# Performance work log

Measured on AMD Instinct MI355X. Metric: run time of the kernel, lower is better.

The kernel has to match this reference:

```python
import jax, jax.numpy as jnp
import numpy as np

N_PTS = 262144      # 512x512 coordinate grid
N_HEADS = 16
HID = 256
N_HID_LAYERS = 3
IN_F = 2
OUT_F = 3
PE_L = 10                  # NeRF positional-encoding frequencies
PE_DIM = 2 * IN_F * PE_L   # sin+cos per freq per coord = 40
CAP = N_PTS // N_HEADS     # balanced partition: points per head


def positional_encoding(x):
    # x: [..., IN_F] -> [..., PE_DIM]
    freqs = (2.0 ** jnp.arange(PE_L, dtype=x.dtype)) * jnp.pi          # [L]
    ang = x[..., None, :] * freqs[:, None]                              # [..., L, IN_F]
    pe = jnp.concatenate([jnp.sin(ang), jnp.cos(ang)], axis=-1)        # [..., L, 2*IN_F]
    return pe.reshape(*x.shape[:-1], PE_DIM)


def setup_inputs() -> dict:
    key = jax.random.key(0)
    ks = jax.random.split(key, 5)
    # Balanced random segment map (equivalent to the module's segment_weight),
    # converted to the static routing table the torch loop recomputes each step:
    # head_idx[h] = where(segment_weight == h)
    rng = np.random.default_rng(0)
    seg = rng.permutation(np.arange(N_PTS) % N_HEADS)
    head_idx = np.stack([np.where(seg == h)[0] for h in range(N_HEADS)]).astype(np.int32)  # [H, CAP]

    coords = jax.random.uniform(ks[0], (1, N_PTS, IN_F), minval=-1.0, maxval=1.0)

    def he(k, shape, fan_in):
        return jax.random.normal(k, shape, dtype=jnp.float32) * np.float32(np.sqrt(2.0 / fan_in))

    W_in = he(ks[1], (N_HEADS, PE_DIM, HID), PE_DIM)
    b_in = jnp.zeros((N_HEADS, HID), jnp.float32)
    W_hid = he(ks[2], (N_HEADS, N_HID_LAYERS, HID, HID), HID)
    b_hid = jnp.zeros((N_HEADS, N_HID_LAYERS, HID), jnp.float32)
    W_out = he(ks[3], (N_HEADS, HID, OUT_F), HID)
    b_out = jnp.zeros((N_HEADS, OUT_F), jnp.float32)

    return dict(coords=coords, head_idx=jnp.asarray(head_idx),
                W_in=W_in, b_in=b_in, W_hid=W_hid, b_hid=b_hid,
                W_out=W_out, b_out=b_out)


def reference(coords, head_idx, W_in, b_in, W_hid, b_hid, W_out, b_out):
    # --- dispatch: gather each head's points (torch: coords[:, index, :]) ---
    coords_h = coords[0][head_idx]                                      # [H, CAP, IN_F]
    # --- per-head MLP (relu_MLP with positional embedding) ---
    h = jax.nn.relu(jnp.einsum('hcd,hdf->hcf', positional_encoding(coords_h), W_in)
                    + b_in[:, None, :])                                 # [H, CAP, HID]
    for l in range(N_HID_LAYERS):
        h = jax.nn.relu(jnp.einsum('hcf,hfg->hcg', h, W_hid[:, l])
                        + b_hid[:, l, None, :])
    out_h = jnp.einsum('hcf,hfo->hco', h, W_out) + b_out[:, None, :]    # [H, CAP, OUT_F]
    # --- combine: scatter per-head outputs back (torch: output_final[0, index, :] = out) ---
    out_final = jnp.zeros((1, N_PTS, OUT_F), coords.dtype)
    out_final = out_final.at[0, head_idx.reshape(-1)].set(out_h.reshape(-1, OUT_F))
    return (out_final, coords)
```

## Files before the change

kernel.cpp:

```cpp
#include <hip/hip_runtime.h>

typedef unsigned short u16;
typedef unsigned int   u32;
typedef __bf16  bf16x8 __attribute__((ext_vector_type(8)));
typedef float   f32x16 __attribute__((ext_vector_type(16)));

#define CAP      16384
#define L0Q_ELS  3072
#define L0_ELS   (4*L0Q_ELS)
#define HID_ELS  (256*256)
#define OUT_ELS  (16*512)
#define HEAD_WS  (L0_ELS + 3*HID_ELS + OUT_ELS)
#define HID_OFF  L0_ELS
#define OUT_OFF  (L0_ELS + 3*HID_ELS)
#define HEAD_CH  (HEAD_WS/8)

union F8 { u32 u[4]; bf16x8 v; };

__device__ __forceinline__ u16 f2b(float f) {
  u32 u = __float_as_uint(f); u += 0x7fffu + ((u >> 16) & 1u); return (u16)(u >> 16);
}
__device__ __forceinline__ u32 packbf2(float a, float b) {
  u32 ua = __float_as_uint(a); ua += 0x7fffu + ((ua >> 16) & 1u);
  u32 ub = __float_as_uint(b); ub += 0x7fffu + ((ub >> 16) & 1u);
  return (ua >> 16) | (ub & 0xffff0000u);
}

__device__ __forceinline__ f32x16 mfma16(bf16x8 a, bf16x8 b, f32x16 c) {
  return __builtin_amdgcn_mfma_f32_32x32x16_bf16(a, b, c, 0, 0, 0);
}

__device__ __forceinline__ void stage_async(const u16* __restrict__ g, short* l,
                                            int bytes, int tid) {
  for (int base = tid * 16; base < bytes; base += 4096)
    __builtin_amdgcn_global_load_lds(
        (const __attribute__((address_space(1))) u32*)((const char*)g + base),
        (__attribute__((address_space(3))) u32*)((char*)l + base), 16, 0, 0);
}

__device__ __forceinline__ bf16x8 fragL0(const short* sl, int i, int t, int lane) {
  return *(const bf16x8*)((const char*)sl + ((i*3 + t) << 10) + (lane << 4));
}
__device__ __forceinline__ bf16x8 fragH(const short* sl, int i, int t, int lane) {
  return *(const bf16x8*)((const char*)sl + ((i*16 + t) << 10) + (lane << 4));
}

__device__ __forceinline__ void load_bias_raw(const float* b, int r, int hh, float4 o[4]) {
#pragma unroll
  for (int g = 0; g < 4; ++g) o[g] = *(const float4*)(b + 32*r + 8*g + 4*hh);
}
__device__ __forceinline__ f32x16 bias_to_acc(const float4 raw[4]) {
  f32x16 a;
#pragma unroll
  for (int g = 0; g < 4; ++g) {
    a[4*g+0] = raw[g].x; a[4*g+1] = raw[g].y;
    a[4*g+2] = raw[g].z; a[4*g+3] = raw[g].w;
  }
  return a;
}

__device__ __forceinline__ void epilogue(f32x16 c, int hh, F8& t0, F8& t1) {
  u32 P[8];
#pragma unroll
  for (int i = 0; i < 8; ++i)
    P[i] = packbf2(fmaxf(c[2*i], 0.f), fmaxf(c[2*i+1], 0.f));
  u32 s0 = hh ? P[0] : P[2], s1 = hh ? P[1] : P[3];
  u32 s2 = hh ? P[4] : P[6], s3 = hh ? P[5] : P[7];
  u32 x0 = __shfl_xor(s0, 32, 64), x1 = __shfl_xor(s1, 32, 64);
  u32 x2 = __shfl_xor(s2, 32, 64), x3 = __shfl_xor(s3, 32, 64);
  t0.u[0] = hh ? x0 : P[0]; t0.u[1] = hh ? x1 : P[1];
  t0.u[2] = hh ? P[2] : x0; t0.u[3] = hh ? P[3] : x1;
  t1.u[0] = hh ? x2 : P[4]; t1.u[1] = hh ? x3 : P[5];
  t1.u[2] = hh ? P[6] : x2; t1.u[3] = hh ? P[7] : x3;
}

__global__ void prep(const float* __restrict__ W_in, const float* __restrict__ b_in,
                     const float* __restrict__ W_hid, const float* __restrict__ W_out,
                     u16* __restrict__ ws,
                     const uint4* __restrict__ csrc, uint4* __restrict__ cdst) {
  const int b = blockIdx.x, tid = threadIdx.x;
  if (b >= 1696) {
    const int i = (b - 1696) * 256 + tid;
    cdst[i] = csrc[i];
    return;
  }
  const int ct = b * 256 + tid;
  const int head = ct / HEAD_CH;
  const int r = ct - head * HEAD_CH;
  u16 v[8];
  if (r < 1536) {
    const int Q = r / 384, rr = r - Q * 384;
    const int f = rr >> 6, ll = rr & 63;
    const int i = (f >= 3) ? 1 : 0, t = f - 3 * i;
    const int hh = ll >> 5, n2 = ll & 31;
    const int kb = 8 * (2 * t + hh), nn = Q * 64 + i * 32 + n2;
#pragma unroll
    for (int j = 0; j < 8; ++j) {
      const int k = kb + j;
      v[j] = (k < 40) ? f2b(W_in[head * 10240 + k * 256 + nn])
           : (k == 40) ? f2b(b_in[head * 256 + nn]) : (u16)0;
    }
  } else if (r < 26112) {
    const int r2 = r - 1536;
    const int l = r2 >> 13, q2 = r2 & 8191;
    const int Q = q2 >> 11, rr = q2 & 2047;
    const int f = rr >> 6, ll = rr & 63;
    const int i = f >> 4, t = f & 15;
    const int hh = ll >> 5, n2 = ll & 31;
    const int kb = 8 * (2 * t + hh), nn = Q * 64 + i * 32 + n2;
    const float* src = W_hid + head * 196608 + l * 65536 + nn;
#pragma unroll
    for (int j = 0; j < 8; ++j)
      v[j] = f2b(src[(kb + j) * 256]);
  } else {
    const int r3 = r - 26112;
    const int t = r3 >> 6, ll = r3 & 63;
    const int hh = ll >> 5, n2 = ll & 31;
    const int kb = 8 * (2 * t + hh);
#pragma unroll
    for (int j = 0; j < 8; ++j)
      v[j] = (n2 < 3) ? f2b(W_out[head * 768 + (kb + j) * 3 + n2]) : (u16)0;
  }
  uint4 o;
  o.x = (u32)v[0] | ((u32)v[1] << 16); o.y = (u32)v[2] | ((u32)v[3] << 16);
  o.z = (u32)v[4] | ((u32)v[5] << 16); o.w = (u32)v[6] | ((u32)v[7] << 16);
  *(uint4*)(ws + (long)ct * 8) = o;
}

__launch_bounds__(256, 2)
__global__ void mlp_main(const float* __restrict__ coords, const int* __restrict__ head_idx,
                         const float* __restrict__ b_hid, const float* __restrict__ b_out,
                         const u16* __restrict__ ws, float* __restrict__ out) {
  __shared__ short ring[2 * 16384];
  const int tid = threadIdx.x;
  const int lane = tid & 63, wv = tid >> 6;
  const int n = lane & 31, hh = lane >> 5;
  const int head = blockIdx.x & 15, chunk = blockIdx.x >> 4;
  const u16* wsh = ws + head * HEAD_WS;

  stage_async(wsh + 0*L0Q_ELS, ring,          6144, tid);
  stage_async(wsh + 1*L0Q_ELS, ring + 16384,  6144, tid);

  const int pt = chunk*128 + wv*32 + n;
  const int g  = head_idx[head*CAP + pt];
  const float2 cxy = *(const float2*)(coords + 2*g);
  const float xs = cxy.x, ys = cxy.y;
  const float bo0 = b_out[head*3+0], bo1 = b_out[head*3+1], bo2 = b_out[head*3+2];

  F8 pe[3];
#pragma unroll
  for (int t = 0; t < 3; ++t) {
    float e[8];
#pragma unroll
    for (int half = 0; half < 2; ++half) {
      const int l = 4*t + 2*hh + half;
      if (l < 10) {
        const float fr = 3.14159265358979323846f * (float)(1 << l);
        float s1, c1, s2, c2;
        sincosf(xs * fr, &s1, &c1);
        sincosf(ys * fr, &s2, &c2);
        e[4*half+0] = s1; e[4*half+1] = s2; e[4*half+2] = c1; e[4*half+3] = c2;
      } else {
        e[4*half+0] = (l == 10) ? 1.0f : 0.0f;
        e[4*half+1] = 0.f; e[4*half+2] = 0.f; e[4*half+3] = 0.f;
      }
    }
    pe[t].u[0] = packbf2(e[0], e[1]); pe[t].u[1] = packbf2(e[2], e[3]);
    pe[t].u[2] = packbf2(e[4], e[5]); pe[t].u[3] = packbf2(e[6], e[7]);
  }

  F8 act0[16], act1[16];
  __syncthreads();

#pragma unroll
  for (int rp = 0; rp < 4; ++rp) {
    short* sl = ring + (rp & 1) * 16384;
    f32x16 acc0 = (f32x16)0.f, acc1 = (f32x16)0.f;
    __builtin_amdgcn_s_setprio(1);
#pragma unroll
    for (int t = 0; t < 3; ++t) {
      acc0 = mfma16(fragL0(sl, 0, t, lane), pe[t].v, acc0);
      acc1 = mfma16(fragL0(sl, 1, t, lane), pe[t].v, acc1);
    }
    __builtin_amdgcn_s_setprio(0);
    __syncthreads();
    const u16* src = (rp < 2) ? (wsh + (rp + 2)*L0Q_ELS) : (wsh + HID_OFF + (rp - 2)*16384);
    const int bytes = (rp < 2) ? 6144 : 32768;
    stage_async(src, sl, bytes, tid);
    epilogue(acc0, hh, act0[4*rp+0], act0[4*rp+1]);
    epilogue(acc1, hh, act0[4*rp+2], act0[4*rp+3]);
  }

  auto hid_layer = [&](const float* bias, F8 (&ain)[16], F8 (&aout)[16],
                       const u16* j0, const u16* j1, const u16* j2, const u16* j3,
                       int b2, int b3) {
    float4 bc0[4], bc1[4], bn0[4], bn1[4];
    load_bias_raw(bias, 0, hh, bc0); load_bias_raw(bias, 1, hh, bc1);
    const u16* jsrc[4] = { j0, j1, j2, j3 };
    const int  jb[4]   = { 32768, 32768, b2, b3 };
#pragma unroll
    for (int rp = 0; rp < 4; ++rp) {
      short* sl = ring + (rp & 1) * 16384;
      if (rp < 3) { load_bias_raw(bias, 2*rp+2, hh, bn0); load_bias_raw(bias, 2*rp+3, hh, bn1); }
      f32x16 acc0 = bias_to_acc(bc0);
      f32x16 acc1 = bias_to_acc(bc1);
      __builtin_amdgcn_s_setprio(1);
#pragma unroll
      for (int t = 0; t < 16; ++t) {
        bf16x8 a0 = fragH(sl, 0, t, lane);
        bf16x8 a1 = fragH(sl, 1, t, lane);
        acc0 = mfma16(a0, ain[t].v, acc0);
        acc1 = mfma16(a1, ain[t].v, acc1);
      }
      __builtin_amdgcn_s_setprio(0);
      __syncthreads();
      if (jb[rp] > 0) stage_async(jsrc[rp], sl, jb[rp], tid);
      epilogue(acc0, hh, aout[4*rp+0], aout[4*rp+1]);
      epilogue(acc1, hh, aout[4*rp+2], aout[4*rp+3]);
      if (rp < 3) {
#pragma unroll
        for (int q = 0; q < 4; ++q) { bc0[q] = bn0[q]; bc1[q] = bn1[q]; }
      }
    }
  };

  const u16* hb = wsh + HID_OFF;
  hid_layer(b_hid + (head*3+0)*256, act0, act1,
            hb + 2*16384, hb + 3*16384, hb + HID_ELS, hb + HID_ELS + 16384, 32768, 32768);
  hid_layer(b_hid + (head*3+1)*256, act1, act0,
            hb + HID_ELS + 2*16384, hb + HID_ELS + 3*16384,
            hb + 2*HID_ELS, hb + 2*HID_ELS + 16384, 32768, 32768);
  hid_layer(b_hid + (head*3+2)*256, act0, act1,
            hb + 2*HID_ELS + 2*16384, hb + 2*HID_ELS + 3*16384,
            wsh + OUT_OFF, (const u16*)0, 16384, 0);

  f32x16 acc = (f32x16)0.f;
  __builtin_amdgcn_s_setprio(1);
#pragma unroll
  for (int t = 0; t < 16; ++t)
    acc = mfma16(fragH(ring, 0, t, lane), act1[t].v, acc);
  __builtin_amdgcn_s_setprio(0);
  if (hh == 0) {
    const long base = (long)g * 3;
    out[base + 0] = acc[0] + bo0;
    out[base + 1] = acc[1] + bo1;
    out[base + 2] = acc[2] + bo2;
  }
}

extern "C" void kernel_launch(void* const* d_in, const int* in_sizes, int n_in,
                              void* d_out, int out_size, void* d_ws, size_t ws_size,
                              hipStream_t stream) {
  const float* coords   = (const float*)d_in[0];
  const int*   head_idx = (const int*)d_in[1];
  const float* W_in     = (const float*)d_in[2];
  const float* b_in     = (const float*)d_in[3];
  const float* W_hid    = (const float*)d_in[4];
  const float* b_hid    = (const float*)d_in[5];
  const float* W_out    = (const float*)d_in[6];
  const float* b_out    = (const float*)d_in[7];
  float* out = (float*)d_out;
  u16*   ws  = (u16*)d_ws;
  if (ws_size < (size_t)HEAD_WS * 16 * sizeof(u16)) return;

  prep<<<dim3(2208), dim3(256), 0, stream>>>(W_in, b_in, W_hid, W_out, ws,
                                             (const uint4*)coords, (uint4*)(out + 786432));
  mlp_main<<<dim3(2048), dim3(256), 0, stream>>>(coords, head_idx, b_hid, b_out, ws, out);
}
```

Before: 206.1 us.

## Process two point tiles per wave to reuse weight fragments, halve block size

Each wave now handles 64 points as two 32-point MFMA tiles that share every weight fragment read from LDS, which halves LDS weight traffic per point. Blocks shrink to 128 threads (2 waves) with launch bounds of 1, and the async staging stride changes to match. The bias is added in the epilogue instead of preloading it into the accumulators. The cost is roughly double the accumulator and activation registers per wave (four 16-entry activation arrays), which lowers occupancy and gives fewer waves to hide latency.

```diff
diff --git a/kernel.cpp b/kernel.cpp
--- a/kernel.cpp
+++ b/kernel.cpp
@@ -32,7 +32,7 @@
 
 __device__ __forceinline__ void stage_async(const u16* __restrict__ g, short* l,
                                             int bytes, int tid) {
-  for (int base = tid * 16; base < bytes; base += 4096)
+  for (int base = tid * 16; base < bytes; base += 2048)
     __builtin_amdgcn_global_load_lds(
         (const __attribute__((address_space(1))) u32*)((const char*)g + base),
         (__attribute__((address_space(3))) u32*)((char*)l + base), 16, 0, 0);
@@ -48,15 +48,6 @@
 __device__ __forceinline__ void load_bias_raw(const float* b, int r, int hh, float4 o[4]) {
 #pragma unroll
   for (int g = 0; g < 4; ++g) o[g] = *(const float4*)(b + 32*r + 8*g + 4*hh);
-}
-__device__ __forceinline__ f32x16 bias_to_acc(const float4 raw[4]) {
-  f32x16 a;
-#pragma unroll
-  for (int g = 0; g < 4; ++g) {
-    a[4*g+0] = raw[g].x; a[4*g+1] = raw[g].y;
-    a[4*g+2] = raw[g].z; a[4*g+3] = raw[g].w;
-  }
-  return a;
 }
 
 __device__ __forceinline__ void epilogue(f32x16 c, int hh, F8& t0, F8& t1) {
@@ -73,6 +64,25 @@
   t1.u[0] = hh ? x2 : P[4]; t1.u[1] = hh ? x3 : P[5];
   t1.u[2] = hh ? P[6] : x2; t1.u[3] = hh ? P[7] : x3;
 }
+__device__ __forceinline__ void epilogue_b(f32x16 c, const float4 bb[4], int hh, F8& t0, F8& t1) {
+  u32 P[8];
+  P[0] = packbf2(fmaxf(c[0]  + bb[0].x, 0.f), fmaxf(c[1]  + bb[0].y, 0.f));
+  P[1] = packbf2(fmaxf(c[2]  + bb[0].z, 0.f), fmaxf(c[3]  + bb[0].w, 0.f));
+  P[2] = packbf2(fmaxf(c[4]  + bb[1].x, 0.f), fmaxf(c[5]  + bb[1].y, 0.f));
+  P[3] = packbf2(fmaxf(c[6]  + bb[1].z, 0.f), fmaxf(c[7]  + bb[1].w, 0.f));
+  P[4] = packbf2(fmaxf(c[8]  + bb[2].x, 0.f), fmaxf(c[9]  + bb[2].y, 0.f));
+  P[5] = packbf2(fmaxf(c[10] + bb[2].z, 0.f), fmaxf(c[11] + bb[2].w, 0.f));
+  P[6] = packbf2(fmaxf(c[12] + bb[3].x, 0.f), fmaxf(c[13] + bb[3].y, 0.f));
+  P[7] = packbf2(fmaxf(c[14] + bb[3].z, 0.f), fmaxf(c[15] + bb[3].w, 0.f));
+  u32 s0 = hh ? P[0] : P[2], s1 = hh ? P[1] : P[3];
+  u32 s2 = hh ? P[4] : P[6], s3 = hh ? P[5] : P[7];
+  u32 x0 = __shfl_xor(s0, 32, 64), x1 = __shfl_xor(s1, 32, 64);
+  u32 x2 = __shfl_xor(s2, 32, 64), x3 = __shfl_xor(s3, 32, 64);
+  t0.u[0] = hh ? x0 : P[0]; t0.u[1] = hh ? x1 : P[1];
+  t0.u[2] = hh ? P[2] : x0; t0.u[3] = hh ? P[3] : x1;
+  t1.u[0] = hh ? x2 : P[4]; t1.u[1] = hh ? x3 : P[5];
+  t1.u[2] = hh ? P[6] : x2; t1.u[3] = hh ? P[7] : x3;
+}
 
 __global__ void prep(const float* __restrict__ W_in, const float* __restrict__ b_in,
                      const float* __restrict__ W_hid, const float* __restrict__ W_out,
@@ -127,7 +137,7 @@
   *(uint4*)(ws + (long)ct * 8) = o;
 }
 
-__launch_bounds__(256, 2)
+__launch_bounds__(128, 1)
 __global__ void mlp_main(const float* __restrict__ coords, const int* __restrict__ head_idx,
                          const float* __restrict__ b_hid, const float* __restrict__ b_out,
                          const u16* __restrict__ ws, float* __restrict__ out) {
@@ -141,110 +151,128 @@
   stage_async(wsh + 0*L0Q_ELS, ring,          6144, tid);
   stage_async(wsh + 1*L0Q_ELS, ring + 16384,  6144, tid);
 
-  const int pt = chunk*128 + wv*32 + n;
-  const int g  = head_idx[head*CAP + pt];
-  const float2 cxy = *(const float2*)(coords + 2*g);
-  const float xs = cxy.x, ys = cxy.y;
+  const int pt = chunk*128 + wv*64 + n;
+  const int g0 = head_idx[head*CAP + pt];
+  const int g1 = head_idx[head*CAP + pt + 32];
+  const float2 c0 = *(const float2*)(coords + 2*g0);
+  const float2 c1 = *(const float2*)(coords + 2*g1);
   const float bo0 = b_out[head*3+0], bo1 = b_out[head*3+1], bo2 = b_out[head*3+2];
 
-  F8 pe[3];
-#pragma unroll
-  for (int t = 0; t < 3; ++t) {
-    float e[8];
-#pragma unroll
-    for (int half = 0; half < 2; ++half) {
-      const int l = 4*t + 2*hh + half;
-      if (l < 10) {
-        const float fr = 3.14159265358979323846f * (float)(1 << l);
-        float s1, c1, s2, c2;
-        sincosf(xs * fr, &s1, &c1);
-        sincosf(ys * fr, &s2, &c2);
-        e[4*half+0] = s1; e[4*half+1] = s2; e[4*half+2] = c1; e[4*half+3] = c2;
-      } else {
-        e[4*half+0] = (l == 10) ? 1.0f : 0.0f;
-        e[4*half+1] = 0.f; e[4*half+2] = 0.f; e[4*half+3] = 0.f;
+  auto build_pe = [&](float xs, float ys, F8 (&pe)[3]) {
+#pragma unroll
+    for (int t = 0; t < 3; ++t) {
+      float e[8];
+#pragma unroll
+      for (int half = 0; half < 2; ++half) {
+        const int l = 4*t + 2*hh + half;
+        if (l < 10) {
+          const float fr = 3.14159265358979323846f * (float)(1 << l);
+          float s1, cc1, s2, cc2;
+          sincosf(xs * fr, &s1, &cc1);
+          sincosf(ys * fr, &s2, &cc2);
+          e[4*half+0] = s1; e[4*half+1] = s2; e[4*half+2] = cc1; e[4*half+3] = cc2;
+        } else {
+          e[4*half+0] = (l == 10) ? 1.0f : 0.0f;
+          e[4*half+1] = 0.f; e[4*half+2] = 0.f; e[4*half+3] = 0.f;
+        }
       }
-    }
-    pe[t].u[0] = packbf2(e[0], e[1]); pe[t].u[1] = packbf2(e[2], e[3]);
-    pe[t].u[2] = packbf2(e[4], e[5]); pe[t].u[3] = packbf2(e[6], e[7]);
-  }
-
-  F8 act0[16], act1[16];
+      pe[t].u[0] = packbf2(e[0], e[1]); pe[t].u[1] = packbf2(e[2], e[3]);
+      pe[t].u[2] = packbf2(e[4], e[5]); pe[t].u[3] = packbf2(e[6], e[7]);
+    }
+  };
+  F8 peA[3], peB[3];
+  build_pe(c0.x, c0.y, peA);
+  build_pe(c1.x, c1.y, peB);
+
+  F8 s0a[16], s0b[16], s1a[16], s1b[16];
   __syncthreads();
 
 #pragma unroll
   for (int rp = 0; rp < 4; ++rp) {
     short* sl = ring + (rp & 1) * 16384;
-    f32x16 acc0 = (f32x16)0.f, acc1 = (f32x16)0.f;
+    f32x16 a00 = (f32x16)0.f, a01 = (f32x16)0.f, a10 = (f32x16)0.f, a11 = (f32x16)0.f;
     __builtin_amdgcn_s_setprio(1);
 #pragma unroll
     for (int t = 0; t < 3; ++t) {
-      acc0 = mfma16(fragL0(sl, 0, t, lane), pe[t].v, acc0);
-      acc1 = mfma16(fragL0(sl, 1, t, lane), pe[t].v, acc1);
+      bf16x8 w0 = fragL0(sl, 0, t, lane);
+      bf16x8 w1 = fragL0(sl, 1, t, lane);
+      a00 = mfma16(w0, peA[t].v, a00);
+      a01 = mfma16(w0, peB[t].v, a01);
+      a10 = mfma16(w1, peA[t].v, a10);
+      a11 = mfma16(w1, peB[t].v, a11);
     }
     __builtin_amdgcn_s_setprio(0);
     __syncthreads();
     const u16* src = (rp < 2) ? (wsh + (rp + 2)*L0Q_ELS) : (wsh + HID_OFF + (rp - 2)*16384);
     const int bytes = (rp < 2) ? 6144 : 32768;
     stage_async(src, sl, bytes, tid);
-    epilogue(acc0, hh, act0[4*rp+0], act0[4*rp+1]);
-    epilogue(acc1, hh, act0[4*rp+2], act0[4*rp+3]);
-  }
-
-  auto hid_layer = [&](const float* bias, F8 (&ain)[16], F8 (&aout)[16],
+    epilogue(a00, hh, s0a[4*rp+0], s0a[4*rp+1]);
+    epilogue(a10, hh, s0a[4*rp+2], s0a[4*rp+3]);
+    epilogue(a01, hh, s0b[4*rp+0], s0b[4*rp+1]);
+    epilogue(a11, hh, s0b[4*rp+2], s0b[4*rp+3]);
+  }
+
+  auto hid_layer = [&](const float* bias, F8 (&ina)[16], F8 (&inb)[16],
+                       F8 (&outa)[16], F8 (&outb)[16],
                        const u16* j0, const u16* j1, const u16* j2, const u16* j3,
                        int b2, int b3) {
-    float4 bc0[4], bc1[4], bn0[4], bn1[4];
-    load_bias_raw(bias, 0, hh, bc0); load_bias_raw(bias, 1, hh, bc1);
     const u16* jsrc[4] = { j0, j1, j2, j3 };
     const int  jb[4]   = { 32768, 32768, b2, b3 };
 #pragma unroll
     for (int rp = 0; rp < 4; ++rp) {
       short* sl = ring + (rp & 1) * 16384;
-      if (rp < 3) { load_bias_raw(bias, 2*rp+2, hh, bn0); load_bias_raw(bias, 2*rp+3, hh, bn1); }
-      f32x16 acc0 = bias_to_acc(bc0);
-      f32x16 acc1 = bias_to_acc(bc1);
+      float4 br0[4], br1[4];
+      load_bias_raw(bias, 2*rp+0, hh, br0);
+      load_bias_raw(bias, 2*rp+1, hh, br1);
+      f32x16 a00 = (f32x16)0.f, a01 = (f32x16)0.f, a10 = (f32x16)0.f, a11 = (f32x16)0.f;
       __builtin_amdgcn_s_setprio(1);
 #pragma unroll
       for (int t = 0; t < 16; ++t) {
-        bf16x8 a0 = fragH(sl, 0, t, lane);
-        bf16x8 a1 = fragH(sl, 1, t, lane);
-        acc0 = mfma16(a0, ain[t].v, acc0);
-        acc1 = mfma16(a1, ain[t].v, acc1);
+        bf16x8 w0 = fragH(sl, 0, t, lane);
+        bf16x8 w1 = fragH(sl, 1, t, lane);
+        a00 = mfma16(w0, ina[t].v, a00);
+        a01 = mfma16(w0, inb[t].v, a01);
+        a10 = mfma16(w1, ina[t].v, a10);
+        a11 = mfma16(w1, inb[t].v, a11);
       }
       __builtin_amdgcn_s_setprio(0);
       __syncthreads();
       if (jb[rp] > 0) stage_async(jsrc[rp], sl, jb[rp], tid);
-      epilogue(acc0, hh, aout[4*rp+0], aout[4*rp+1]);
-      epilogue(acc1, hh, aout[4*rp+2], aout[4*rp+3]);
-      if (rp < 3) {
-#pragma unroll
-        for (int q = 0; q < 4; ++q) { bc0[q] = bn0[q]; bc1[q] = bn1[q]; }
-      }
+      epilogue_b(a00, br0, hh, outa[4*rp+0], outa[4*rp+1]);
+      epilogue_b(a10, br1, hh, outa[4*rp+2], outa[4*rp+3]);
+      epilogue_b(a01, br0, hh, outb[4*rp+0], outb[4*rp+1]);
+      epilogue_b(a11, br1, hh, outb[4*rp+2], outb[4*rp+3]);
     }
   };
 
   const u16* hb = wsh + HID_OFF;
-  hid_layer(b_hid + (head*3+0)*256, act0, act1,
+  hid_layer(b_hid + (head*3+0)*256, s0a, s0b, s1a, s1b,
             hb + 2*16384, hb + 3*16384, hb + HID_ELS, hb + HID_ELS + 16384, 32768, 32768);
-  hid_layer(b_hid + (head*3+1)*256, act1, act0,
+  hid_layer(b_hid + (head*3+1)*256, s1a, s1b, s0a, s0b,
             hb + HID_ELS + 2*16384, hb + HID_ELS + 3*16384,
             hb + 2*HID_ELS, hb + 2*HID_ELS + 16384, 32768, 32768);
-  hid_layer(b_hid + (head*3+2)*256, act0, act1,
+  hid_layer(b_hid + (head*3+2)*256, s0a, s0b, s1a, s1b,
             hb + 2*HID_ELS + 2*16384, hb + 2*HID_ELS + 3*16384,
             wsh + OUT_OFF, (const u16*)0, 16384, 0);
 
-  f32x16 acc = (f32x16)0.f;
+  f32x16 o0 = (f32x16)0.f, o1 = (f32x16)0.f;
   __builtin_amdgcn_s_setprio(1);
 #pragma unroll
-  for (int t = 0; t < 16; ++t)
-    acc = mfma16(fragH(ring, 0, t, lane), act1[t].v, acc);
+  for (int t = 0; t < 16; ++t) {
+    bf16x8 w = fragH(ring, 0, t, lane);
+    o0 = mfma16(w, s1a[t].v, o0);
+    o1 = mfma16(w, s1b[t].v, o1);
+  }
   __builtin_amdgcn_s_setprio(0);
   if (hh == 0) {
-    const long base = (long)g * 3;
-    out[base + 0] = acc[0] + bo0;
-    out[base + 1] = acc[1] + bo1;
-    out[base + 2] = acc[2] + bo2;
+    const long b0 = (long)g0 * 3;
+    out[b0 + 0] = o0[0] + bo0;
+    out[b0 + 1] = o0[1] + bo1;
+    out[b0 + 2] = o0[2] + bo2;
+    const long b1 = (long)g1 * 3;
+    out[b1 + 0] = o1[0] + bo0;
+    out[b1 + 1] = o1[1] + bo1;
+    out[b1 + 2] = o1[2] + bo2;
   }
 }
 
@@ -265,5 +293,5 @@
 
   prep<<<dim3(2208), dim3(256), 0, stream>>>(W_in, b_in, W_hid, W_out, ws,
                                              (const uint4*)coords, (uint4*)(out + 786432));
-  mlp_main<<<dim3(2048), dim3(256), 0, stream>>>(coords, head_idx, b_hid, b_out, ws, out);
-}
+  mlp_main<<<dim3(2048), dim3(128), 0, stream>>>(coords, head_idx, b_hid, b_out, ws, out);
+}
```

Result: slower. 273.6 us (+32.7%).
